# Kernel tuning notes

Measured on AMD Instinct MI355X. Metric: run time of the kernel, lower is better.

## Reference

```python
import jax, jax.numpy as jnp
import numpy as np

N_NODES = 20000
N_EDGES = 160000
F_IN = 512
HIDDEN = 512
N_CLASSES = 40


def setup_inputs() -> dict:
    key = jax.random.key(0)
    k1, k2, k3, k4 = jax.random.split(key, 4)
    x = jax.random.normal(k1, (N_NODES, F_IN), dtype=jnp.float32)
    edge_index = jax.random.randint(k2, (2, N_EDGES), 0, N_NODES, dtype=jnp.int64)
    # Glorot-ish init scale for the linear weights
    W1 = jax.random.normal(k3, (F_IN, HIDDEN), dtype=jnp.float32) / np.sqrt(F_IN)
    b1 = jnp.zeros((HIDDEN,), dtype=jnp.float32)
    W2 = jax.random.normal(k4, (HIDDEN, N_CLASSES), dtype=jnp.float32) / np.sqrt(HIDDEN)
    b2 = jnp.zeros((N_CLASSES,), dtype=jnp.float32)
    return {"x": x, "edge_index": edge_index, "W1": W1, "b1": b1, "W2": W2, "b2": b2}


def _gcn_conv(x, W, b, src, dst, n_nodes):
    """PyG GCNConv: h = D^-1/2 (A+I) D^-1/2 (x W) + b, self-loops already in src/dst."""
    h = x @ W  # [N, out]
    deg = jax.ops.segment_sum(jnp.ones_like(dst, dtype=h.dtype), dst, num_segments=n_nodes)
    deg_inv_sqrt = jnp.where(deg > 0, jax.lax.rsqrt(jnp.maximum(deg, 1.0)), 0.0)
    norm = deg_inv_sqrt[src] * deg_inv_sqrt[dst]  # [E]
    msg = h[src] * norm[:, None]  # [E, out]
    return jax.ops.segment_sum(msg, dst, num_segments=n_nodes) + b


def reference(x, edge_index, W1, b1, W2, b2):
    n = x.shape[0]
    loop = jnp.arange(n, dtype=edge_index.dtype)
    src = jnp.concatenate([edge_index[0], loop])  # add self-loops
    dst = jnp.concatenate([edge_index[1], loop])
    h = _gcn_conv(x, W1, b1, src, dst, n)
    h = jax.nn.relu(h)
    # dropout(p=0.5) is identity in eval mode
    out = _gcn_conv(h, W2, b2, src, dst, n)
    return out
```

## Files before the change

### kernel.cpp

```cpp
#include <hip/hip_runtime.h>
#include <hip/hip_bf16.h>
#include <stdint.h>

#define N_NODES  20000
#define N_EDGES  160000
#define N_CLS    40
#define M_PAD    20096
#define CNT_PAD  20480
#define CAP      64

typedef __bf16 bf16;
typedef __attribute__((ext_vector_type(8))) __bf16 bf16x8;
typedef __attribute__((ext_vector_type(4))) float floatx4;

__device__ inline floatx4 zero4() { floatx4 z = {0.f, 0.f, 0.f, 0.f}; return z; }

typedef __attribute__((address_space(3))) uint32_t lds_u32;
typedef __attribute__((address_space(1))) const uint32_t glb_u32;
__device__ inline void ldst16(const bf16* g, bf16* l) {
    __builtin_amdgcn_global_load_lds((glb_u32*)g, (lds_u32*)l, 16, 0, 0);
}

struct Params {
    const float* x; const int* ei; const float* W1; const float* b1;
    const float* W2; const float* b2; float* out;
    bf16 *xb, *w1t, *w2p, *h1, *a1; float* h2;
    int *cnt, *colb;
};

#define S0_ZERO 20
#define S0_CONV 5024
#define S0_W1T  128
#define S0_W2P  96
#define S0_TOT  (S0_ZERO + S0_CONV + S0_W1T + S0_W2P)
#define NB_G1   640
#define NB_FILL 625

__global__ __launch_bounds__(256) void k_s0(Params p) {
    const int vb = blockIdx.x, tid = threadIdx.x;
    if (vb < S0_ZERO) {
        int4* dz = (int4*)(p.cnt) + vb * 256 + tid;
        *dz = make_int4(0, 0, 0, 0);
    } else if (vb < S0_ZERO + S0_CONV) {
        long e0 = ((long)(vb - S0_ZERO) * 256 + tid) * 8;
        int row = (int)(e0 >> 9);
        bf16x8 v;
        if (row < N_NODES) {
            const float4* ptr = (const float4*)(p.x + e0);
            float4 f0 = ptr[0], f1 = ptr[1];
            v[0] = (bf16)f0.x; v[1] = (bf16)f0.y; v[2] = (bf16)f0.z; v[3] = (bf16)f0.w;
            v[4] = (bf16)f1.x; v[5] = (bf16)f1.y; v[6] = (bf16)f1.z; v[7] = (bf16)f1.w;
        } else {
            for (int j = 0; j < 8; ++j) v[j] = (bf16)0.f;
        }
        *(bf16x8*)(p.xb + e0) = v;
    } else if (vb < S0_ZERO + S0_CONV + S0_W1T) {
        int t  = (vb - S0_ZERO - S0_CONV) * 256 + tid;
        int n  = t & 511;
        int k0 = (t >> 9) * 8;
        bf16x8 v;
        for (int j = 0; j < 8; ++j) v[j] = (bf16)p.W1[((k0 + j) << 9) + n];
        *(bf16x8*)(p.w1t + n * 512 + k0) = v;
    } else {
        int t = (vb - S0_ZERO - S0_CONV - S0_W1T) * 256 + tid;
        int j = t & 7; int e = t >> 3;
        int lane = e & 63; e >>= 6;
        int nb = e % 3; int kt = e / 3;
        int k = kt * 32 + (lane >> 4) * 8 + j;
        int n = nb * 16 + (lane & 15);
        float v = (n < N_CLS) ? p.W2[k * N_CLS + n] : 0.f;
        p.w2p[t] = (bf16)v;
    }
}

__global__ __launch_bounds__(256) void k_g1f(Params p) {
    if (blockIdx.x >= NB_G1) {
        int e = (blockIdx.x - NB_G1) * 256 + threadIdx.x;
        if (e < N_EDGES) {
            int d = p.ei[N_EDGES + e];
            int j = atomicAdd(&p.cnt[d], 1);
            if (j < CAP) p.colb[d * CAP + j] = p.ei[e];
        }
        return;
    }
    const int g  = blockIdx.x;
    const int mi = (g >> 5) * 8 + (g & 7);
    const int ni = (g >> 3) & 3;
    if (mi >= 157) return;
    __shared__ bf16 As[2][128 * 32];
    __shared__ bf16 Bs[2][128 * 32];
    const int tid  = threadIdx.x;
    const int lane = tid & 63;
    const int w    = tid >> 6;
    const int wm   = w >> 1, wn = w & 1;
    const int m0   = mi * 128;
    const int n0   = ni * 128;
    const int fr   = lane & 15, fq = lane >> 4;

    floatx4 acc[4][4];
    for (int mb = 0; mb < 4; ++mb)
        for (int nb = 0; nb < 4; ++nb) acc[mb][nb] = zero4();

    const int sr = lane >> 2;
    const int sk = (lane & 3) * 8;
    const bf16* Ag = p.xb  + (long)(m0 + w * 32 + sr) * 512 + sk;
    const bf16* Bg = p.w1t + (long)(n0 + w * 32 + sr) * 512 + sk;
    const int wof = w * 1024;

    ldst16(Ag,            As[0] + wof);
    ldst16(Ag + 16 * 512, As[0] + wof + 512);
    ldst16(Bg,            Bs[0] + wof);
    ldst16(Bg + 16 * 512, Bs[0] + wof + 512);

    for (int kt = 0; kt < 16; ++kt) {
        const int cur = kt & 1, nxt = cur ^ 1;
        __syncthreads();
        if (kt < 15) {
            const int k1 = (kt + 1) * 32;
            ldst16(Ag + k1,            As[nxt] + wof);
            ldst16(Ag + k1 + 16 * 512, As[nxt] + wof + 512);
            ldst16(Bg + k1,            Bs[nxt] + wof);
            ldst16(Bg + k1 + 16 * 512, Bs[nxt] + wof + 512);
        }
        bf16x8 af[4], bfv[4];
        for (int mb = 0; mb < 4; ++mb)
            af[mb]  = *(const bf16x8*)(As[cur] + (wm * 64 + mb * 16 + fr) * 32 + fq * 8);
        for (int nb = 0; nb < 4; ++nb)
            bfv[nb] = *(const bf16x8*)(Bs[cur] + (wn * 64 + nb * 16 + fr) * 32 + fq * 8);
        for (int mb = 0; mb < 4; ++mb)
            for (int nb = 0; nb < 4; ++nb)
                acc[mb][nb] = __builtin_amdgcn_mfma_f32_16x16x32_bf16(af[mb], bfv[nb], acc[mb][nb], 0, 0, 0);
    }
    for (int mb = 0; mb < 4; ++mb)
        for (int nb = 0; nb < 4; ++nb) {
            int row0 = m0 + wm * 64 + mb * 16 + fq * 4;
            int c    = n0 + wn * 64 + nb * 16 + fr;
            for (int r = 0; r < 4; ++r)
                p.h1[(long)(row0 + r) * 512 + c] = (bf16)acc[mb][nb][r];
        }
}

__global__ __launch_bounds__(256) void k_agg1(Params p) {
    const int i = blockIdx.x * 4 + (threadIdx.x >> 6);
    const int l = threadIdx.x & 63;
    bf16* outp = p.a1 + (long)i * 512 + l * 8;
    if (i >= N_NODES) {
        bf16x8 z;
        for (int j = 0; j < 8; ++j) z[j] = (bf16)0.f;
        *(bf16x8*)outp = z;
        return;
    }
    const int ci = p.cnt[i];
    const float di = rsqrtf((float)(ci + 1));
    float acc[8];
    {
        bf16x8 v = *(const bf16x8*)(p.h1 + (long)i * 512 + l * 8);
        const float wi = di * di;
        for (int j = 0; j < 8; ++j) acc[j] = (float)v[j] * wi;
    }
    const int e1 = ci < CAP ? ci : CAP;
    const int* rowcol = p.colb + (long)i * CAP;
    int e = 0;
    for (; e + 8 <= e1; e += 8) {
        int4 sa = *(const int4*)(rowcol + e);
        int4 sb = *(const int4*)(rowcol + e + 4);
        float wgt[8];
        wgt[0] = rsqrtf((float)(p.cnt[sa.x] + 1)) * di;
        wgt[1] = rsqrtf((float)(p.cnt[sa.y] + 1)) * di;
        wgt[2] = rsqrtf((float)(p.cnt[sa.z] + 1)) * di;
        wgt[3] = rsqrtf((float)(p.cnt[sa.w] + 1)) * di;
        wgt[4] = rsqrtf((float)(p.cnt[sb.x] + 1)) * di;
        wgt[5] = rsqrtf((float)(p.cnt[sb.y] + 1)) * di;
        wgt[6] = rsqrtf((float)(p.cnt[sb.z] + 1)) * di;
        wgt[7] = rsqrtf((float)(p.cnt[sb.w] + 1)) * di;
        bf16x8 u[8];
        u[0] = *(const bf16x8*)(p.h1 + (long)sa.x * 512 + l * 8);
        u[1] = *(const bf16x8*)(p.h1 + (long)sa.y * 512 + l * 8);
        u[2] = *(const bf16x8*)(p.h1 + (long)sa.z * 512 + l * 8);
        u[3] = *(const bf16x8*)(p.h1 + (long)sa.w * 512 + l * 8);
        u[4] = *(const bf16x8*)(p.h1 + (long)sb.x * 512 + l * 8);
        u[5] = *(const bf16x8*)(p.h1 + (long)sb.y * 512 + l * 8);
        u[6] = *(const bf16x8*)(p.h1 + (long)sb.z * 512 + l * 8);
        u[7] = *(const bf16x8*)(p.h1 + (long)sb.w * 512 + l * 8);
        for (int q = 0; q < 8; ++q)
            for (int j = 0; j < 8; ++j) acc[j] += (float)u[q][j] * wgt[q];
    }
    for (; e + 4 <= e1; e += 4) {
        int4 ss = *(const int4*)(rowcol + e);
        float w0 = rsqrtf((float)(p.cnt[ss.x] + 1)) * di;
        float w1 = rsqrtf((float)(p.cnt[ss.y] + 1)) * di;
        float w2 = rsqrtf((float)(p.cnt[ss.z] + 1)) * di;
        float w3 = rsqrtf((float)(p.cnt[ss.w] + 1)) * di;
        bf16x8 u0 = *(const bf16x8*)(p.h1 + (long)ss.x * 512 + l * 8);
        bf16x8 u1 = *(const bf16x8*)(p.h1 + (long)ss.y * 512 + l * 8);
        bf16x8 u2 = *(const bf16x8*)(p.h1 + (long)ss.z * 512 + l * 8);
        bf16x8 u3 = *(const bf16x8*)(p.h1 + (long)ss.w * 512 + l * 8);
        for (int j = 0; j < 8; ++j)
            acc[j] += (float)u0[j] * w0 + (float)u1[j] * w1 + (float)u2[j] * w2 + (float)u3[j] * w3;
    }
    for (; e < e1; ++e) {
        int s = rowcol[e];
        float wt = rsqrtf((float)(p.cnt[s] + 1)) * di;
        bf16x8 u = *(const bf16x8*)(p.h1 + (long)s * 512 + l * 8);
        for (int j = 0; j < 8; ++j) acc[j] += (float)u[j] * wt;
    }
    const float4* bp = (const float4*)(p.b1 + l * 8);
    float4 c0 = bp[0], c1 = bp[1];
    float bb[8] = {c0.x, c0.y, c0.z, c0.w, c1.x, c1.y, c1.z, c1.w};
    bf16x8 o;
    for (int j = 0; j < 8; ++j) {
        float f = acc[j] + bb[j];
        f = f > 0.f ? f : 0.f;
        o[j] = (bf16)f;
    }
    *(bf16x8*)outp = o;
}

__global__ __launch_bounds__(256) void k_gemm2(Params p) {
    const int tid = threadIdx.x, lane = tid & 63, w = tid >> 6;
    const int m0 = blockIdx.x * 64 + w * 16;
    const int fr = lane & 15, fq = lane >> 4;
    const bf16* Ap = p.a1 + (long)(m0 + fr) * 512 + fq * 8;
    floatx4 acc[3];
    for (int nb = 0; nb < 3; ++nb) acc[nb] = zero4();
    for (int kt = 0; kt < 16; ++kt) {
        bf16x8 af = *(const bf16x8*)(Ap + kt * 32);
        for (int nb = 0; nb < 3; ++nb) {
            bf16x8 bfr = *(const bf16x8*)(p.w2p + ((kt * 3 + nb) * 64 + lane) * 8);
            acc[nb] = __builtin_amdgcn_mfma_f32_16x16x32_bf16(af, bfr, acc[nb], 0, 0, 0);
        }
    }
    for (int nb = 0; nb < 3; ++nb)
        for (int r = 0; r < 4; ++r)
            p.h2[(long)(m0 + fq * 4 + r) * 48 + nb * 16 + fr] = acc[nb][r];
}

__global__ __launch_bounds__(256) void k_agg2(Params p) {
    const int i = blockIdx.x * 4 + (threadIdx.x >> 6);
    const int l = threadIdx.x & 63;
    if (i >= N_NODES || l >= N_CLS) return;
    const int ci = p.cnt[i];
    const float di = rsqrtf((float)(ci + 1));
    float acc = p.h2[(long)i * 48 + l] * di * di;
    const int e1 = ci < CAP ? ci : CAP;
    const int* rowcol = p.colb + (long)i * CAP;
    int e = 0;
    for (; e + 4 <= e1; e += 4) {
        int4 ss = *(const int4*)(rowcol + e);
        acc += p.h2[(long)ss.x * 48 + l] * (rsqrtf((float)(p.cnt[ss.x] + 1)) * di)
             + p.h2[(long)ss.y * 48 + l] * (rsqrtf((float)(p.cnt[ss.y] + 1)) * di)
             + p.h2[(long)ss.z * 48 + l] * (rsqrtf((float)(p.cnt[ss.z] + 1)) * di)
             + p.h2[(long)ss.w * 48 + l] * (rsqrtf((float)(p.cnt[ss.w] + 1)) * di);
    }
    for (; e < e1; ++e) {
        int s = rowcol[e];
        acc += p.h2[(long)s * 48 + l] * (rsqrtf((float)(p.cnt[s] + 1)) * di);
    }
    p.out[(long)i * N_CLS + l] = acc + p.b2[l];
}


extern "C" void kernel_launch(void* const* d_in, const int* in_sizes, int n_in,
                              void* d_out, int out_size, void* d_ws, size_t ws_size,
                              hipStream_t stream) {
    Params p;
    p.x  = (const float*)d_in[0];
    p.ei = (const int*)d_in[1];
    p.W1 = (const float*)d_in[2];
    p.b1 = (const float*)d_in[3];
    p.W2 = (const float*)d_in[4];
    p.b2 = (const float*)d_in[5];
    p.out = (float*)d_out;

    char* base = (char*)d_ws;
    size_t o = 0;
    auto alloc = [&](size_t bytes) { size_t r = o; o = (o + bytes + 255) & ~(size_t)255; return r; };
    p.xb   = (bf16*)(base + alloc((size_t)M_PAD * 512 * 2));
    p.w1t  = (bf16*)(base + alloc((size_t)512 * 512 * 2));
    p.w2p  = (bf16*)(base + alloc((size_t)24576 * 2));
    p.h1   = (bf16*)(base + alloc((size_t)M_PAD * 512 * 2));
    p.a1   = (bf16*)(base + alloc((size_t)M_PAD * 512 * 2));
    p.h2   = (float*)(base + alloc((size_t)M_PAD * 48 * 4));
    p.cnt  = (int*)(base + alloc((size_t)CNT_PAD * 4));
    p.colb = (int*)(base + alloc((size_t)N_NODES * CAP * 4));

    k_s0   <<<S0_TOT,           256, 0, stream>>>(p);
    k_g1f  <<<NB_G1 + NB_FILL,  256, 0, stream>>>(p);
    k_agg1 <<<M_PAD / 4,        256, 0, stream>>>(p);
    k_gemm2<<<M_PAD / 64,       256, 0, stream>>>(p);
    k_agg2 <<<N_NODES / 4,      256, 0, stream>>>(p);
}
```

Baseline: 156.9 us.

## Fuse layer-1 aggregation with second GEMM via swizzled LDS tile

Merges the first aggregation kernel and the small second GEMM into one kernel. Each block aggregates 16 nodes into an XOR-swizzled shared-memory tile, then three waves run MFMA against W2 to write h2 directly. This removes the a1 intermediate buffer's write and re-read plus one kernel launch. In exchange each block does 4 nodes per wave serially, so there is less parallelism per block, and one wave sits idle during the GEMM phase.

```diff
diff --git a/kernel.cpp b/kernel.cpp
--- a/kernel.cpp
+++ b/kernel.cpp
@@ -24,7 +24,7 @@
 struct Params {
     const float* x; const int* ei; const float* W1; const float* b1;
     const float* W2; const float* b2; float* out;
-    bf16 *xb, *w1t, *w2p, *h1, *a1; float* h2;
+    bf16 *xb, *w1t, *w2p, *h1; float* h2;
     int *cnt, *colb;
 };
 
@@ -140,99 +140,98 @@
         }
 }
 
-__global__ __launch_bounds__(256) void k_agg1(Params p) {
-    const int i = blockIdx.x * 4 + (threadIdx.x >> 6);
-    const int l = threadIdx.x & 63;
-    bf16* outp = p.a1 + (long)i * 512 + l * 8;
-    if (i >= N_NODES) {
-        bf16x8 z;
-        for (int j = 0; j < 8; ++j) z[j] = (bf16)0.f;
-        *(bf16x8*)outp = z;
-        return;
-    }
-    const int ci = p.cnt[i];
-    const float di = rsqrtf((float)(ci + 1));
-    float acc[8];
-    {
-        bf16x8 v = *(const bf16x8*)(p.h1 + (long)i * 512 + l * 8);
-        const float wi = di * di;
-        for (int j = 0; j < 8; ++j) acc[j] = (float)v[j] * wi;
-    }
-    const int e1 = ci < CAP ? ci : CAP;
-    const int* rowcol = p.colb + (long)i * CAP;
-    int e = 0;
-    for (; e + 8 <= e1; e += 8) {
-        int4 sa = *(const int4*)(rowcol + e);
-        int4 sb = *(const int4*)(rowcol + e + 4);
-        float wgt[8];
-        wgt[0] = rsqrtf((float)(p.cnt[sa.x] + 1)) * di;
-        wgt[1] = rsqrtf((float)(p.cnt[sa.y] + 1)) * di;
-        wgt[2] = rsqrtf((float)(p.cnt[sa.z] + 1)) * di;
-        wgt[3] = rsqrtf((float)(p.cnt[sa.w] + 1)) * di;
-        wgt[4] = rsqrtf((float)(p.cnt[sb.x] + 1)) * di;
-        wgt[5] = rsqrtf((float)(p.cnt[sb.y] + 1)) * di;
-        wgt[6] = rsqrtf((float)(p.cnt[sb.z] + 1)) * di;
-        wgt[7] = rsqrtf((float)(p.cnt[sb.w] + 1)) * di;
-        bf16x8 u[8];
-        u[0] = *(const bf16x8*)(p.h1 + (long)sa.x * 512 + l * 8);
-        u[1] = *(const bf16x8*)(p.h1 + (long)sa.y * 512 + l * 8);
-        u[2] = *(const bf16x8*)(p.h1 + (long)sa.z * 512 + l * 8);
-        u[3] = *(const bf16x8*)(p.h1 + (long)sa.w * 512 + l * 8);
-        u[4] = *(const bf16x8*)(p.h1 + (long)sb.x * 512 + l * 8);
-        u[5] = *(const bf16x8*)(p.h1 + (long)sb.y * 512 + l * 8);
-        u[6] = *(const bf16x8*)(p.h1 + (long)sb.z * 512 + l * 8);
-        u[7] = *(const bf16x8*)(p.h1 + (long)sb.w * 512 + l * 8);
-        for (int q = 0; q < 8; ++q)
-            for (int j = 0; j < 8; ++j) acc[j] += (float)u[q][j] * wgt[q];
-    }
-    for (; e + 4 <= e1; e += 4) {
-        int4 ss = *(const int4*)(rowcol + e);
-        float w0 = rsqrtf((float)(p.cnt[ss.x] + 1)) * di;
-        float w1 = rsqrtf((float)(p.cnt[ss.y] + 1)) * di;
-        float w2 = rsqrtf((float)(p.cnt[ss.z] + 1)) * di;
-        float w3 = rsqrtf((float)(p.cnt[ss.w] + 1)) * di;
-        bf16x8 u0 = *(const bf16x8*)(p.h1 + (long)ss.x * 512 + l * 8);
-        bf16x8 u1 = *(const bf16x8*)(p.h1 + (long)ss.y * 512 + l * 8);
-        bf16x8 u2 = *(const bf16x8*)(p.h1 + (long)ss.z * 512 + l * 8);
-        bf16x8 u3 = *(const bf16x8*)(p.h1 + (long)ss.w * 512 + l * 8);
-        for (int j = 0; j < 8; ++j)
-            acc[j] += (float)u0[j] * w0 + (float)u1[j] * w1 + (float)u2[j] * w2 + (float)u3[j] * w3;
-    }
-    for (; e < e1; ++e) {
-        int s = rowcol[e];
-        float wt = rsqrtf((float)(p.cnt[s] + 1)) * di;
-        bf16x8 u = *(const bf16x8*)(p.h1 + (long)s * 512 + l * 8);
-        for (int j = 0; j < 8; ++j) acc[j] += (float)u[j] * wt;
-    }
+__global__ __launch_bounds__(256) void k_agg1g2(Params p) {
+    __shared__ bf16 t[16 * 512];
+    const int tid = threadIdx.x, l = tid & 63, w = tid >> 6;
+    const int ib = blockIdx.x * 16;
+
     const float4* bp = (const float4*)(p.b1 + l * 8);
     float4 c0 = bp[0], c1 = bp[1];
     float bb[8] = {c0.x, c0.y, c0.z, c0.w, c1.x, c1.y, c1.z, c1.w};
-    bf16x8 o;
-    for (int j = 0; j < 8; ++j) {
-        float f = acc[j] + bb[j];
-        f = f > 0.f ? f : 0.f;
-        o[j] = (bf16)f;
-    }
-    *(bf16x8*)outp = o;
-}
-
-__global__ __launch_bounds__(256) void k_gemm2(Params p) {
-    const int tid = threadIdx.x, lane = tid & 63, w = tid >> 6;
-    const int m0 = blockIdx.x * 64 + w * 16;
-    const int fr = lane & 15, fq = lane >> 4;
-    const bf16* Ap = p.a1 + (long)(m0 + fr) * 512 + fq * 8;
-    floatx4 acc[3];
-    for (int nb = 0; nb < 3; ++nb) acc[nb] = zero4();
-    for (int kt = 0; kt < 16; ++kt) {
-        bf16x8 af = *(const bf16x8*)(Ap + kt * 32);
-        for (int nb = 0; nb < 3; ++nb) {
-            bf16x8 bfr = *(const bf16x8*)(p.w2p + ((kt * 3 + nb) * 64 + lane) * 8);
-            acc[nb] = __builtin_amdgcn_mfma_f32_16x16x32_bf16(af, bfr, acc[nb], 0, 0, 0);
-        }
-    }
-    for (int nb = 0; nb < 3; ++nb)
-        for (int r = 0; r < 4; ++r)
-            p.h2[(long)(m0 + fq * 4 + r) * 48 + nb * 16 + fr] = acc[nb][r];
+
+    for (int q4 = 0; q4 < 4; ++q4) {
+        const int r = w * 4 + q4;
+        const int i = ib + r;
+        bf16x8 o;
+        if (i >= N_NODES) {
+            for (int j = 0; j < 8; ++j) o[j] = (bf16)0.f;
+        } else {
+            const int ci = p.cnt[i];
+            const float di = rsqrtf((float)(ci + 1));
+            float acc[8];
+            {
+                bf16x8 v = *(const bf16x8*)(p.h1 + (long)i * 512 + l * 8);
+                const float wi = di * di;
+                for (int j = 0; j < 8; ++j) acc[j] = (float)v[j] * wi;
+            }
+            const int e1 = ci < CAP ? ci : CAP;
+            const int* rowcol = p.colb + (long)i * CAP;
+            int e = 0;
+            for (; e + 8 <= e1; e += 8) {
+                int4 sa = *(const int4*)(rowcol + e);
+                int4 sb = *(const int4*)(rowcol + e + 4);
+                float wgt[8];
+                wgt[0] = rsqrtf((float)(p.cnt[sa.x] + 1)) * di;
+                wgt[1] = rsqrtf((float)(p.cnt[sa.y] + 1)) * di;
+                wgt[2] = rsqrtf((float)(p.cnt[sa.z] + 1)) * di;
+                wgt[3] = rsqrtf((float)(p.cnt[sa.w] + 1)) * di;
+                wgt[4] = rsqrtf((float)(p.cnt[sb.x] + 1)) * di;
+                wgt[5] = rsqrtf((float)(p.cnt[sb.y] + 1)) * di;
+                wgt[6] = rsqrtf((float)(p.cnt[sb.z] + 1)) * di;
+                wgt[7] = rsqrtf((float)(p.cnt[sb.w] + 1)) * di;
+                bf16x8 u[8];
+                u[0] = *(const bf16x8*)(p.h1 + (long)sa.x * 512 + l * 8);
+                u[1] = *(const bf16x8*)(p.h1 + (long)sa.y * 512 + l * 8);
+                u[2] = *(const bf16x8*)(p.h1 + (long)sa.z * 512 + l * 8);
+                u[3] = *(const bf16x8*)(p.h1 + (long)sa.w * 512 + l * 8);
+                u[4] = *(const bf16x8*)(p.h1 + (long)sb.x * 512 + l * 8);
+                u[5] = *(const bf16x8*)(p.h1 + (long)sb.y * 512 + l * 8);
+                u[6] = *(const bf16x8*)(p.h1 + (long)sb.z * 512 + l * 8);
+                u[7] = *(const bf16x8*)(p.h1 + (long)sb.w * 512 + l * 8);
+                for (int q = 0; q < 8; ++q)
+                    for (int j = 0; j < 8; ++j) acc[j] += (float)u[q][j] * wgt[q];
+            }
+            for (; e + 4 <= e1; e += 4) {
+                int4 ss = *(const int4*)(rowcol + e);
+                float w0 = rsqrtf((float)(p.cnt[ss.x] + 1)) * di;
+                float w1 = rsqrtf((float)(p.cnt[ss.y] + 1)) * di;
+                float w2 = rsqrtf((float)(p.cnt[ss.z] + 1)) * di;
+                float w3 = rsqrtf((float)(p.cnt[ss.w] + 1)) * di;
+                bf16x8 u0 = *(const bf16x8*)(p.h1 + (long)ss.x * 512 + l * 8);
+                bf16x8 u1 = *(const bf16x8*)(p.h1 + (long)ss.y * 512 + l * 8);
+                bf16x8 u2 = *(const bf16x8*)(p.h1 + (long)ss.z * 512 + l * 8);
+                bf16x8 u3 = *(const bf16x8*)(p.h1 + (long)ss.w * 512 + l * 8);
+                for (int j = 0; j < 8; ++j)
+                    acc[j] += (float)u0[j] * w0 + (float)u1[j] * w1 + (float)u2[j] * w2 + (float)u3[j] * w3;
+            }
+            for (; e < e1; ++e) {
+                int s = rowcol[e];
+                float wt = rsqrtf((float)(p.cnt[s] + 1)) * di;
+                bf16x8 u = *(const bf16x8*)(p.h1 + (long)s * 512 + l * 8);
+                for (int j = 0; j < 8; ++j) acc[j] += (float)u[j] * wt;
+            }
+            for (int j = 0; j < 8; ++j) {
+                float f = acc[j] + bb[j];
+                f = f > 0.f ? f : 0.f;
+                o[j] = (bf16)f;
+            }
+        }
+        *(bf16x8*)((char*)t + r * 1024 + ((l * 16) ^ ((r & 7) << 4))) = o;
+    }
+    __syncthreads();
+    if (w < 3) {
+        const int fr = l & 15, fq = l >> 4;
+        const int nb = w;
+        floatx4 acc2 = zero4();
+        for (int kt = 0; kt < 16; ++kt) {
+            bf16x8 af = *(const bf16x8*)((const char*)t + fr * 1024 +
+                                         ((kt * 64 + fq * 16) ^ ((fr & 7) << 4)));
+            bf16x8 bfr = *(const bf16x8*)(p.w2p + ((kt * 3 + nb) * 64 + l) * 8);
+            acc2 = __builtin_amdgcn_mfma_f32_16x16x32_bf16(af, bfr, acc2, 0, 0, 0);
+        }
+        for (int r2 = 0; r2 < 4; ++r2)
+            p.h2[(long)(ib + fq * 4 + r2) * 48 + nb * 16 + fr] = acc2[r2];
+    }
 }
 
 __global__ __launch_bounds__(256) void k_agg2(Params p) {
@@ -279,14 +278,12 @@
     p.w1t  = (bf16*)(base + alloc((size_t)512 * 512 * 2));
     p.w2p  = (bf16*)(base + alloc((size_t)24576 * 2));
     p.h1   = (bf16*)(base + alloc((size_t)M_PAD * 512 * 2));
-    p.a1   = (bf16*)(base + alloc((size_t)M_PAD * 512 * 2));
     p.h2   = (float*)(base + alloc((size_t)M_PAD * 48 * 4));
     p.cnt  = (int*)(base + alloc((size_t)CNT_PAD * 4));
     p.colb = (int*)(base + alloc((size_t)N_NODES * CAP * 4));
 
-    k_s0   <<<S0_TOT,           256, 0, stream>>>(p);
-    k_g1f  <<<NB_G1 + NB_FILL,  256, 0, stream>>>(p);
-    k_agg1 <<<M_PAD / 4,        256, 0, stream>>>(p);
-    k_gemm2<<<M_PAD / 64,       256, 0, stream>>>(p);
-    k_agg2 <<<N_NODES / 4,      256, 0, stream>>>(p);
-}
+    k_s0    <<<S0_TOT,           256, 0, stream>>>(p);
+    k_g1f   <<<NB_G1 + NB_FILL,  256, 0, stream>>>(p);
+    k_agg1g2<<<M_PAD / 16,       256, 0, stream>>>(p);
+    k_agg2  <<<N_NODES / 4,      256, 0, stream>>>(p);
+}
```

Measured after the change: 153.8 us. About the same (-1.9%).
